# Optimization experiments

Measured on AMD Instinct MI355X. Metric: run time of the kernel, lower is better.

The kernel has to match this reference:

```python
import jax, jax.numpy as jnp
import numpy as np

EPS = 1e-8
TEMPERATURE = 1.0


def setup_inputs() -> dict:
    key = jax.random.key(0)
    basin_seq = jax.random.normal(key, (4, 512, 64), dtype=jnp.float32)
    residual_scale = jnp.ones((), dtype=jnp.float32)  # nn.Parameter(torch.tensor(1.0))
    return {"basin_seq": basin_seq, "residual_scale": residual_scale}


def _project_to_simplex(x):
    sp = jax.nn.softplus(x)
    p = sp / (sp.sum(axis=-1, keepdims=True) + EPS)
    return jnp.maximum(p, EPS)


def _qfi_attention_weights(x, temperature):
    # x: (B, T, D)
    p = _project_to_simplex(x)
    # fisher_rao_distance_simplex re-normalizes both operands
    p = p / (p.sum(axis=-1, keepdims=True) + EPS)
    # Faithful: eps is inside the sqrt, so this is a true (B,T,T,D) reduction,
    # not sqrt(p) @ sqrt(p)^T.
    inner = jnp.sqrt(p[:, :, None, :] * p[:, None, :, :] + EPS).sum(axis=-1)  # (B,T,T)
    inner = jnp.clip(inner, -1.0 + 1e-6, 1.0 - 1e-6)
    dist = 2.0 * jnp.arccos(inner)
    logits = -dist / max(float(temperature), 1e-6)
    return jax.nn.softmax(logits, axis=-1)  # (B,T,T)


def _phi_from_activations(acts):
    # acts: (B, T, D)
    t = acts.shape[1]
    x = acts - acts.mean(axis=1, keepdims=True)
    cov = jnp.einsum('btd,bte->bde', x, x) / (t + EPS)
    var = jnp.maximum(jnp.diagonal(cov, axis1=-2, axis2=-1), EPS)  # (B,D)
    denom = jnp.maximum(jnp.sqrt(var[:, :, None] * var[:, None, :]), EPS)
    corr = jnp.clip(cov / denom, -1.0, 1.0)
    d = corr.shape[-1]
    offdiag = corr * (1.0 - jnp.eye(d, dtype=corr.dtype))
    return jnp.abs(offdiag).mean(axis=(-2, -1))  # (B,)


def _kappa_proxy(x):
    return jnp.linalg.norm(x, axis=-1).mean(axis=-1)  # (B,)


def reference(basin_seq, residual_scale):
    x = basin_seq
    for _ in range(2):
        w = _qfi_attention_weights(x, TEMPERATURE)
        x_attn = jnp.einsum('bij,bjd->bid', w, x)
        x = 0.5 * x + 0.5 * x_attn
        x = x + 0.01 * residual_scale * (x_attn - x)
    phi = _phi_from_activations(x)
    kappa = _kappa_proxy(x)
    return (x, phi, kappa)
```

## Files before the change

kernel.cpp:

```cpp
#include <hip/hip_runtime.h>
#include <math.h>

#define B_ 4
#define T_ 512
#define D_ 64
#define EPS 1e-8f

__device__ __forceinline__ float wave_sum(float v) {
#pragma unroll
  for (int m = 1; m < 64; m <<= 1) v += __shfl_xor(v, m, 64);
  return v;
}
__device__ __forceinline__ float wave_max(float v) {
#pragma unroll
  for (int m = 1; m < 64; m <<= 1) v = fmaxf(v, __shfl_xor(v, m, 64));
  return v;
}
__device__ __forceinline__ float softplus_f(float x) {
  return fmaxf(x, 0.0f) + log1pf(expf(-fabsf(x)));
}

__global__ __launch_bounds__(256) void proj_kernel(const float* __restrict__ x,
                                                   float* __restrict__ s) {
  int wave = threadIdx.x >> 6, lane = threadIdx.x & 63;
  int row = blockIdx.x * 4 + wave;
  float sp = softplus_f(x[row * D_ + lane]);
  float s1 = wave_sum(sp);
  float p = sp / (s1 + EPS);
  p = fmaxf(p, EPS);
  float s2 = wave_sum(p);
  s[row * D_ + lane] = sqrtf(p / (s2 + EPS));
}

__global__ __launch_bounds__(256) void logits_kernel(const float* __restrict__ s,
                                                     float* __restrict__ L) {
  int jt = blockIdx.x, it = blockIdx.y, b = blockIdx.z;
  __shared__ float si[64][68];
  __shared__ float sj[64][68];
  int tid = threadIdx.x;
  const float* sb = s + b * T_ * D_;
#pragma unroll
  for (int k = 0; k < 4; ++k) {
    int idx = tid + k * 256;
    int row = idx >> 4, c4 = idx & 15;
    *(float4*)&si[row][c4 * 4] = *(const float4*)(sb + (it * 64 + row) * D_ + c4 * 4);
    *(float4*)&sj[row][c4 * 4] = *(const float4*)(sb + (jt * 64 + row) * D_ + c4 * 4);
  }
  __syncthreads();

  int i4 = tid >> 4, j4 = tid & 15;
  float acc[4][4];
#pragma unroll
  for (int a = 0; a < 4; ++a)
#pragma unroll
    for (int c = 0; c < 4; ++c) acc[a][c] = 0.f;

#pragma unroll 4
  for (int d4 = 0; d4 < 16; ++d4) {
    float4 A[4], Bv[4];
#pragma unroll
    for (int a = 0; a < 4; ++a) A[a] = *(const float4*)&si[i4 + 16 * a][d4 * 4];
#pragma unroll
    for (int c = 0; c < 4; ++c) Bv[c] = *(const float4*)&sj[j4 + 16 * c][d4 * 4];
#pragma unroll
    for (int a = 0; a < 4; ++a)
#pragma unroll
      for (int c = 0; c < 4; ++c) {
        acc[a][c] = fmaf(A[a].x, Bv[c].x, acc[a][c]);
        acc[a][c] = fmaf(A[a].y, Bv[c].y, acc[a][c]);
        acc[a][c] = fmaf(A[a].z, Bv[c].z, acc[a][c]);
        acc[a][c] = fmaf(A[a].w, Bv[c].w, acc[a][c]);
      }
  }
#pragma unroll
  for (int a = 0; a < 4; ++a) {
    int i = it * 64 + i4 + 16 * a;
    float* Lr = L + ((size_t)(b * T_) + i) * T_ + jt * 64;
#pragma unroll
    for (int c = 0; c < 4; ++c) {
      float inner = fminf(fmaxf(acc[a][c], -1.0f + 1e-6f), 1.0f - 1e-6f);
      Lr[j4 + 16 * c] = -2.0f * acosf(inner);
    }
  }
}

__global__ __launch_bounds__(256) void apply_kernel(const float* __restrict__ L,
                                                    const float* __restrict__ xin,
                                                    const float* __restrict__ rsp,
                                                    float* __restrict__ xout,
                                                    float* __restrict__ sout) {
  int b = blockIdx.y;
  int i0 = blockIdx.x * 8;
  __shared__ float wR[8][512];
  __shared__ float red[4][8][64];
  int tid = threadIdx.x;
  int w = tid >> 6, lane = tid & 63;

#pragma unroll
  for (int r = 0; r < 2; ++r) {
    int i = w * 2 + r;
    const float* Lr = L + ((size_t)(b * T_) + i0 + i) * T_;
    float4 v0 = ((const float4*)Lr)[lane];
    float4 v1 = ((const float4*)Lr)[64 + lane];
    float m = fmaxf(fmaxf(fmaxf(v0.x, v0.y), fmaxf(v0.z, v0.w)),
                    fmaxf(fmaxf(v1.x, v1.y), fmaxf(v1.z, v1.w)));
    m = wave_max(m);
    float4 e0, e1;
    e0.x = __expf(v0.x - m); e0.y = __expf(v0.y - m);
    e0.z = __expf(v0.z - m); e0.w = __expf(v0.w - m);
    e1.x = __expf(v1.x - m); e1.y = __expf(v1.y - m);
    e1.z = __expf(v1.z - m); e1.w = __expf(v1.w - m);
    float ssum = wave_sum(e0.x + e0.y + e0.z + e0.w + e1.x + e1.y + e1.z + e1.w);
    float inv = 1.0f / ssum;
    e0.x *= inv; e0.y *= inv; e0.z *= inv; e0.w *= inv;
    e1.x *= inv; e1.y *= inv; e1.z *= inv; e1.w *= inv;
    *(float4*)&wR[i][lane * 4] = e0;
    *(float4*)&wR[i][256 + lane * 4] = e1;
  }
  __syncthreads();

  int dg = tid & 15, js = tid >> 4;
  float acc[8][4];
#pragma unroll
  for (int i = 0; i < 8; ++i)
#pragma unroll
    for (int k = 0; k < 4; ++k) acc[i][k] = 0.f;

  const float* xb = xin + (size_t)(b * T_) * D_;
#pragma unroll 2
  for (int jj = 0; jj < 8; ++jj) {
    int jbase = jj * 64 + js * 4;
    float xr[4][4];
#pragma unroll
    for (int c = 0; c < 4; ++c) {
      float4 xv = *(const float4*)(xb + (jbase + c) * D_ + dg * 4);
      xr[c][0] = xv.x; xr[c][1] = xv.y; xr[c][2] = xv.z; xr[c][3] = xv.w;
    }
#pragma unroll
    for (int i = 0; i < 8; ++i) {
      float4 wv = *(const float4*)&wR[i][jbase];
      float wc[4] = {wv.x, wv.y, wv.z, wv.w};
#pragma unroll
      for (int c = 0; c < 4; ++c)
#pragma unroll
        for (int k = 0; k < 4; ++k)
          acc[i][k] = fmaf(wc[c], xr[c][k], acc[i][k]);
    }
  }

#pragma unroll
  for (int i = 0; i < 8; ++i)
#pragma unroll
    for (int k = 0; k < 4; ++k) {
      float v = acc[i][k];
      v += __shfl_xor(v, 16, 64);
      v += __shfl_xor(v, 32, 64);
      acc[i][k] = v;
    }
  if (lane < 16) {
#pragma unroll
    for (int i = 0; i < 8; ++i)
      *(float4*)&red[w][i][lane * 4] =
          make_float4(acc[i][0], acc[i][1], acc[i][2], acc[i][3]);
  }
  __syncthreads();

  float c01 = 0.01f * rsp[0];
#pragma unroll
  for (int h = 0; h < 2; ++h) {
    int i = w + 4 * h, d = lane;
    float xa = red[0][i][d] + red[1][i][d] + red[2][i][d] + red[3][i][d];
    size_t idx = ((size_t)(b * T_) + i0 + i) * D_ + d;
    float xn = 0.5f * (1.0f - c01) * xin[idx] + 0.5f * (1.0f + c01) * xa;
    xout[idx] = xn;
    float sp = softplus_f(xn);
    float s1 = wave_sum(sp);
    float p = sp / (s1 + EPS);
    p = fmaxf(p, EPS);
    float s2 = wave_sum(p);
    sout[idx] = sqrtf(p / (s2 + EPS));
  }
}

__global__ __launch_bounds__(256) void p1_kernel(const float* __restrict__ x,
                                                 float* __restrict__ covp,
                                                 float* __restrict__ meanp,
                                                 float* __restrict__ kappap) {
  int blk = blockIdx.x;
  int b = blk >> 3, sl = blk & 7;
  const float* xb = x + ((size_t)(b * T_) + sl * 64) * D_;
  __shared__ float tile[64][68];
  __shared__ float red2[4][64];
  __shared__ float kred[4];
  int tid = threadIdx.x;
#pragma unroll
  for (int k = 0; k < 4; ++k) {
    int idx = tid + k * 256;
    int row = idx >> 4, c4 = idx & 15;
    *(float4*)&tile[row][c4 * 4] = *(const float4*)(xb + row * D_ + c4 * 4);
  }
  __syncthreads();

  {
    int d = tid & 63, q = tid >> 6;
    float ms = 0.f;
#pragma unroll
    for (int tt = 0; tt < 16; ++tt) ms += tile[q * 16 + tt][d];
    red2[q][d] = ms;
  }

  {
    int tr = tid >> 2, qq = tid & 3;
    float ksq = 0.f;
#pragma unroll
    for (int k = 0; k < 16; ++k) {
      float v = tile[tr][qq * 16 + k];
      ksq = fmaf(v, v, ksq);
    }
    ksq += __shfl_xor(ksq, 1, 64);
    ksq += __shfl_xor(ksq, 2, 64);
    float contrib = (qq == 0) ? sqrtf(ksq) : 0.f;
    contrib = wave_sum(contrib);
    if ((tid & 63) == 0) kred[tid >> 6] = contrib;
  }

  int dd = tid >> 2, e16 = tid & 3;
  float acc[16];
#pragma unroll
  for (int k = 0; k < 16; ++k) acc[k] = 0.f;
  for (int tt = 0; tt < 64; ++tt) {
    float xd = tile[tt][dd];
    const float4* te = (const float4*)&tile[tt][e16 * 16];
    float4 v0 = te[0], v1 = te[1], v2 = te[2], v3 = te[3];
    acc[0]  = fmaf(xd, v0.x, acc[0]);  acc[1]  = fmaf(xd, v0.y, acc[1]);
    acc[2]  = fmaf(xd, v0.z, acc[2]);  acc[3]  = fmaf(xd, v0.w, acc[3]);
    acc[4]  = fmaf(xd, v1.x, acc[4]);  acc[5]  = fmaf(xd, v1.y, acc[5]);
    acc[6]  = fmaf(xd, v1.z, acc[6]);  acc[7]  = fmaf(xd, v1.w, acc[7]);
    acc[8]  = fmaf(xd, v2.x, acc[8]);  acc[9]  = fmaf(xd, v2.y, acc[9]);
    acc[10] = fmaf(xd, v2.z, acc[10]); acc[11] = fmaf(xd, v2.w, acc[11]);
    acc[12] = fmaf(xd, v3.x, acc[12]); acc[13] = fmaf(xd, v3.y, acc[13]);
    acc[14] = fmaf(xd, v3.z, acc[14]); acc[15] = fmaf(xd, v3.w, acc[15]);
  }
  float* cp = covp + (size_t)blk * 4096 + dd * 64 + e16 * 16;
#pragma unroll
  for (int kk = 0; kk < 4; ++kk)
    *(float4*)(cp + kk * 4) =
        make_float4(acc[kk * 4], acc[kk * 4 + 1], acc[kk * 4 + 2], acc[kk * 4 + 3]);
  __syncthreads();
  if (tid < 64)
    meanp[blk * 64 + tid] = red2[0][tid] + red2[1][tid] + red2[2][tid] + red2[3][tid];
  if (tid == 0) kappap[blk] = kred[0] + kred[1] + kred[2] + kred[3];
}

__global__ __launch_bounds__(256) void p2_kernel(const float* __restrict__ covp,
                                                 const float* __restrict__ meanp,
                                                 const float* __restrict__ kappap,
                                                 float* __restrict__ out) {
  int b = blockIdx.x;
  __shared__ float mu[64];
  __shared__ float var[64];
  __shared__ float phired[4];
  int tid = threadIdx.x;
  if (tid < 64) {
    float m = 0.f;
#pragma unroll
    for (int s = 0; s < 8; ++s) m += meanp[(b * 8 + s) * 64 + tid];
    mu[tid] = m * (1.0f / 512.0f);
  }
  __syncthreads();

  int dd = tid >> 2, e16 = tid & 3;
  float acc[16];
#pragma unroll
  for (int k = 0; k < 16; ++k) acc[k] = 0.f;
#pragma unroll
  for (int s = 0; s < 8; ++s) {
    const float* cp = covp + (size_t)(b * 8 + s) * 4096 + dd * 64 + e16 * 16;
#pragma unroll
    for (int kk = 0; kk < 4; ++kk) {
      float4 v = *(const float4*)(cp + kk * 4);
      acc[kk * 4] += v.x; acc[kk * 4 + 1] += v.y;
      acc[kk * 4 + 2] += v.z; acc[kk * 4 + 3] += v.w;
    }
  }
  float mud = mu[dd];
#pragma unroll
  for (int k = 0; k < 16; ++k)
    acc[k] = acc[k] * (1.0f / 512.0f) - mud * mu[e16 * 16 + k];
  if ((dd >> 4) == e16) var[dd] = fmaxf(acc[dd & 15], EPS);
  __syncthreads();

  float vd = var[dd];
  float psum = 0.f;
#pragma unroll
  for (int k = 0; k < 16; ++k) {
    int e = e16 * 16 + k;
    if (e == dd) continue;
    float denom = fmaxf(sqrtf(vd * var[e]), EPS);
    float cc = fminf(fmaxf(acc[k] / denom, -1.0f), 1.0f);
    psum += fabsf(cc);
  }
  psum = wave_sum(psum);
  if ((tid & 63) == 0) phired[tid >> 6] = psum;
  __syncthreads();
  if (tid == 0) {
    out[B_ * T_ * D_ + b] = (phired[0] + phired[1] + phired[2] + phired[3]) *
                            (1.0f / 4096.0f);
    float ks = 0.f;
#pragma unroll
    for (int s = 0; s < 8; ++s) ks += kappap[b * 8 + s];
    out[B_ * T_ * D_ + B_ + b] = ks * (1.0f / 512.0f);
  }
}

extern "C" void kernel_launch(void* const* d_in, const int* in_sizes, int n_in,
                              void* d_out, int out_size, void* d_ws, size_t ws_size,
                              hipStream_t stream) {
  const float* x0 = (const float*)d_in[0];
  const float* rs = (const float*)d_in[1];
  float* out = (float*)d_out;
  float* s     = (float*)d_ws;
  float* L     = s + B_ * T_ * D_;
  float* x1    = L + B_ * T_ * T_;
  float* covp  = x1 + B_ * T_ * D_;
  float* meanp = covp + 32 * 4096;
  float* kappap = meanp + 32 * 64;

  dim3 lgrd(8, 8, 4), agrd(64, 4);
  proj_kernel<<<(B_ * T_) / 4, 256, 0, stream>>>(x0, s);
  logits_kernel<<<lgrd, 256, 0, stream>>>(s, L);
  apply_kernel<<<agrd, 256, 0, stream>>>(L, x0, rs, x1, s);
  logits_kernel<<<lgrd, 256, 0, stream>>>(s, L);
  apply_kernel<<<agrd, 256, 0, stream>>>(L, x1, rs, out, s);
  p1_kernel<<<32, 256, 0, stream>>>(out, covp, meanp, kappap);
  p2_kernel<<<4, 256, 0, stream>>>(covp, meanp, kappap, out);
}
```

Baseline: 104.3 us.

## Fuse logits computation into attention apply kernel and fold stats into second pass

Each attention block now computes its own 8x512 logits tile in shared memory and no longer writes or reads the B×T×T logits buffer in global memory. That removes the separate logits launches and their global round-trip. The second attention pass also emits per-block covariance, mean and norm partials, which removes the p1 kernel. In exchange, each block recomputes the s_j loads for the full sequence, only 256 blocks are launched, and p2 must now reduce 64 partials instead of 8. A separate s2 buffer avoids a read/write race on s.

```diff
diff --git a/kernel.cpp b/kernel.cpp
--- a/kernel.cpp
+++ b/kernel.cpp
@@ -32,76 +32,94 @@
   s[row * D_ + lane] = sqrtf(p / (s2 + EPS));
 }
 
-__global__ __launch_bounds__(256) void logits_kernel(const float* __restrict__ s,
-                                                     float* __restrict__ L) {
-  int jt = blockIdx.x, it = blockIdx.y, b = blockIdx.z;
-  __shared__ float si[64][68];
-  __shared__ float sj[64][68];
-  int tid = threadIdx.x;
-  const float* sb = s + b * T_ * D_;
-#pragma unroll
-  for (int k = 0; k < 4; ++k) {
-    int idx = tid + k * 256;
-    int row = idx >> 4, c4 = idx & 15;
-    *(float4*)&si[row][c4 * 4] = *(const float4*)(sb + (it * 64 + row) * D_ + c4 * 4);
-    *(float4*)&sj[row][c4 * 4] = *(const float4*)(sb + (jt * 64 + row) * D_ + c4 * 4);
-  }
-  __syncthreads();
-
-  int i4 = tid >> 4, j4 = tid & 15;
-  float acc[4][4];
-#pragma unroll
-  for (int a = 0; a < 4; ++a)
-#pragma unroll
-    for (int c = 0; c < 4; ++c) acc[a][c] = 0.f;
-
-#pragma unroll 4
-  for (int d4 = 0; d4 < 16; ++d4) {
-    float4 A[4], Bv[4];
-#pragma unroll
-    for (int a = 0; a < 4; ++a) A[a] = *(const float4*)&si[i4 + 16 * a][d4 * 4];
-#pragma unroll
-    for (int c = 0; c < 4; ++c) Bv[c] = *(const float4*)&sj[j4 + 16 * c][d4 * 4];
-#pragma unroll
-    for (int a = 0; a < 4; ++a)
-#pragma unroll
-      for (int c = 0; c < 4; ++c) {
-        acc[a][c] = fmaf(A[a].x, Bv[c].x, acc[a][c]);
-        acc[a][c] = fmaf(A[a].y, Bv[c].y, acc[a][c]);
-        acc[a][c] = fmaf(A[a].z, Bv[c].z, acc[a][c]);
-        acc[a][c] = fmaf(A[a].w, Bv[c].w, acc[a][c]);
-      }
-  }
-#pragma unroll
-  for (int a = 0; a < 4; ++a) {
-    int i = it * 64 + i4 + 16 * a;
-    float* Lr = L + ((size_t)(b * T_) + i) * T_ + jt * 64;
-#pragma unroll
-    for (int c = 0; c < 4; ++c) {
-      float inner = fminf(fmaxf(acc[a][c], -1.0f + 1e-6f), 1.0f - 1e-6f);
-      Lr[j4 + 16 * c] = -2.0f * acosf(inner);
-    }
-  }
-}
-
-__global__ __launch_bounds__(256) void apply_kernel(const float* __restrict__ L,
-                                                    const float* __restrict__ xin,
-                                                    const float* __restrict__ rsp,
-                                                    float* __restrict__ xout,
-                                                    float* __restrict__ sout) {
-  int b = blockIdx.y;
-  int i0 = blockIdx.x * 8;
-  __shared__ float wR[8][512];
-  __shared__ float red[4][8][64];
+template <bool PART>
+__global__ __launch_bounds__(256) void attn_kernel(
+    const float* __restrict__ s_in, const float* __restrict__ x_in,
+    const float* __restrict__ rsp, float* __restrict__ x_out,
+    float* __restrict__ s_out, float* __restrict__ covp,
+    float* __restrict__ meanp, float* __restrict__ kappap) {
+  int b = blockIdx.y, ic = blockIdx.x;
+  int i0 = ic * 8;
+  __shared__ __align__(16) float smem[13352];
+  float* si8 = smem;
+  float* wbuf = smem + 544;
+  float* sj = smem + 4640;
+  float* red = sj;
+  float* xf = sj + 2048;
+  float* kred = sj + 2592;
   int tid = threadIdx.x;
   int w = tid >> 6, lane = tid & 63;
+  const float* sb = s_in + (size_t)b * T_ * D_;
+  const float* xb = x_in + (size_t)b * T_ * D_;
+
+#pragma unroll
+  for (int k = 0; k < 2; ++k) {
+    int idx = tid + k * 256, r = idx >> 6, d = idx & 63;
+    si8[r * 68 + d] = sb[(i0 + r) * D_ + d];
+  }
+  __syncthreads();
+
+  int iq = tid >> 7, jq = (tid >> 2) & 31, ds = tid & 3;
+  float4 Areg[4][4];
+#pragma unroll
+  for (int a = 0; a < 4; ++a)
+#pragma unroll
+    for (int dq = 0; dq < 4; ++dq)
+      Areg[a][dq] = *(const float4*)&si8[(iq * 4 + a) * 68 + ds * 16 + dq * 4];
+
+  for (int c = 0; c < 4; ++c) {
+    __syncthreads();
+#pragma unroll
+    for (int k = 0; k < 8; ++k) {
+      int idx = tid + k * 256, r = idx >> 4, q = idx & 15;
+      *(float4*)&sj[r * 68 + q * 4] =
+          *(const float4*)(sb + (c * 128 + r) * D_ + q * 4);
+    }
+    __syncthreads();
+    float accL[4][4];
+#pragma unroll
+    for (int a = 0; a < 4; ++a)
+#pragma unroll
+      for (int cc = 0; cc < 4; ++cc) accL[a][cc] = 0.f;
+#pragma unroll
+    for (int dq = 0; dq < 4; ++dq) {
+      float4 Bv[4];
+#pragma unroll
+      for (int cc = 0; cc < 4; ++cc)
+        Bv[cc] = *(const float4*)&sj[(jq + 32 * cc) * 68 + ds * 16 + dq * 4];
+#pragma unroll
+      for (int a = 0; a < 4; ++a) {
+        float4 A = Areg[a][dq];
+#pragma unroll
+        for (int cc = 0; cc < 4; ++cc) {
+          accL[a][cc] = fmaf(A.x, Bv[cc].x, accL[a][cc]);
+          accL[a][cc] = fmaf(A.y, Bv[cc].y, accL[a][cc]);
+          accL[a][cc] = fmaf(A.z, Bv[cc].z, accL[a][cc]);
+          accL[a][cc] = fmaf(A.w, Bv[cc].w, accL[a][cc]);
+        }
+      }
+    }
+#pragma unroll
+    for (int a = 0; a < 4; ++a)
+#pragma unroll
+      for (int cc = 0; cc < 4; ++cc) {
+        float v = accL[a][cc];
+        v += __shfl_xor(v, 1, 64);
+        v += __shfl_xor(v, 2, 64);
+        if (ds == 0) {
+          float inner = fminf(fmaxf(v, -1.0f + 1e-6f), 1.0f - 1e-6f);
+          wbuf[(iq * 4 + a) * 512 + c * 128 + jq + 32 * cc] = -2.0f * acosf(inner);
+        }
+      }
+  }
+  __syncthreads();
 
 #pragma unroll
   for (int r = 0; r < 2; ++r) {
     int i = w * 2 + r;
-    const float* Lr = L + ((size_t)(b * T_) + i0 + i) * T_;
-    float4 v0 = ((const float4*)Lr)[lane];
-    float4 v1 = ((const float4*)Lr)[64 + lane];
+    float* Wr = wbuf + i * 512;
+    float4 v0 = ((float4*)Wr)[lane];
+    float4 v1 = ((float4*)Wr)[64 + lane];
     float m = fmaxf(fmaxf(fmaxf(v0.x, v0.y), fmaxf(v0.z, v0.w)),
                     fmaxf(fmaxf(v1.x, v1.y), fmaxf(v1.z, v1.w)));
     m = wave_max(m);
@@ -114,8 +132,8 @@
     float inv = 1.0f / ssum;
     e0.x *= inv; e0.y *= inv; e0.z *= inv; e0.w *= inv;
     e1.x *= inv; e1.y *= inv; e1.z *= inv; e1.w *= inv;
-    *(float4*)&wR[i][lane * 4] = e0;
-    *(float4*)&wR[i][256 + lane * 4] = e1;
+    ((float4*)Wr)[lane] = e0;
+    ((float4*)Wr)[64 + lane] = e1;
   }
   __syncthreads();
 
@@ -125,8 +143,6 @@
   for (int i = 0; i < 8; ++i)
 #pragma unroll
     for (int k = 0; k < 4; ++k) acc[i][k] = 0.f;
-
-  const float* xb = xin + (size_t)(b * T_) * D_;
 #pragma unroll 2
   for (int jj = 0; jj < 8; ++jj) {
     int jbase = jj * 64 + js * 4;
@@ -138,7 +154,7 @@
     }
 #pragma unroll
     for (int i = 0; i < 8; ++i) {
-      float4 wv = *(const float4*)&wR[i][jbase];
+      float4 wv = *(const float4*)&wbuf[i * 512 + jbase];
       float wc[4] = {wv.x, wv.y, wv.z, wv.w};
 #pragma unroll
       for (int c = 0; c < 4; ++c)
@@ -147,7 +163,6 @@
           acc[i][k] = fmaf(wc[c], xr[c][k], acc[i][k]);
     }
   }
-
 #pragma unroll
   for (int i = 0; i < 8; ++i)
 #pragma unroll
@@ -160,96 +175,68 @@
   if (lane < 16) {
 #pragma unroll
     for (int i = 0; i < 8; ++i)
-      *(float4*)&red[w][i][lane * 4] =
+      *(float4*)&red[(w * 8 + i) * 64 + lane * 4] =
           make_float4(acc[i][0], acc[i][1], acc[i][2], acc[i][3]);
   }
   __syncthreads();
 
   float c01 = 0.01f * rsp[0];
+  float kacc = 0.f;
 #pragma unroll
   for (int h = 0; h < 2; ++h) {
     int i = w + 4 * h, d = lane;
-    float xa = red[0][i][d] + red[1][i][d] + red[2][i][d] + red[3][i][d];
+    float xa = red[(0 * 8 + i) * 64 + d] + red[(1 * 8 + i) * 64 + d] +
+               red[(2 * 8 + i) * 64 + d] + red[(3 * 8 + i) * 64 + d];
     size_t idx = ((size_t)(b * T_) + i0 + i) * D_ + d;
-    float xn = 0.5f * (1.0f - c01) * xin[idx] + 0.5f * (1.0f + c01) * xa;
-    xout[idx] = xn;
-    float sp = softplus_f(xn);
-    float s1 = wave_sum(sp);
-    float p = sp / (s1 + EPS);
-    p = fmaxf(p, EPS);
-    float s2 = wave_sum(p);
-    sout[idx] = sqrtf(p / (s2 + EPS));
-  }
-}
-
-__global__ __launch_bounds__(256) void p1_kernel(const float* __restrict__ x,
-                                                 float* __restrict__ covp,
-                                                 float* __restrict__ meanp,
-                                                 float* __restrict__ kappap) {
-  int blk = blockIdx.x;
-  int b = blk >> 3, sl = blk & 7;
-  const float* xb = x + ((size_t)(b * T_) + sl * 64) * D_;
-  __shared__ float tile[64][68];
-  __shared__ float red2[4][64];
-  __shared__ float kred[4];
-  int tid = threadIdx.x;
-#pragma unroll
-  for (int k = 0; k < 4; ++k) {
-    int idx = tid + k * 256;
-    int row = idx >> 4, c4 = idx & 15;
-    *(float4*)&tile[row][c4 * 4] = *(const float4*)(xb + row * D_ + c4 * 4);
-  }
-  __syncthreads();
-
-  {
-    int d = tid & 63, q = tid >> 6;
-    float ms = 0.f;
-#pragma unroll
-    for (int tt = 0; tt < 16; ++tt) ms += tile[q * 16 + tt][d];
-    red2[q][d] = ms;
-  }
-
-  {
-    int tr = tid >> 2, qq = tid & 3;
-    float ksq = 0.f;
-#pragma unroll
-    for (int k = 0; k < 16; ++k) {
-      float v = tile[tr][qq * 16 + k];
-      ksq = fmaf(v, v, ksq);
-    }
-    ksq += __shfl_xor(ksq, 1, 64);
-    ksq += __shfl_xor(ksq, 2, 64);
-    float contrib = (qq == 0) ? sqrtf(ksq) : 0.f;
-    contrib = wave_sum(contrib);
-    if ((tid & 63) == 0) kred[tid >> 6] = contrib;
-  }
-
-  int dd = tid >> 2, e16 = tid & 3;
-  float acc[16];
-#pragma unroll
-  for (int k = 0; k < 16; ++k) acc[k] = 0.f;
-  for (int tt = 0; tt < 64; ++tt) {
-    float xd = tile[tt][dd];
-    const float4* te = (const float4*)&tile[tt][e16 * 16];
-    float4 v0 = te[0], v1 = te[1], v2 = te[2], v3 = te[3];
-    acc[0]  = fmaf(xd, v0.x, acc[0]);  acc[1]  = fmaf(xd, v0.y, acc[1]);
-    acc[2]  = fmaf(xd, v0.z, acc[2]);  acc[3]  = fmaf(xd, v0.w, acc[3]);
-    acc[4]  = fmaf(xd, v1.x, acc[4]);  acc[5]  = fmaf(xd, v1.y, acc[5]);
-    acc[6]  = fmaf(xd, v1.z, acc[6]);  acc[7]  = fmaf(xd, v1.w, acc[7]);
-    acc[8]  = fmaf(xd, v2.x, acc[8]);  acc[9]  = fmaf(xd, v2.y, acc[9]);
-    acc[10] = fmaf(xd, v2.z, acc[10]); acc[11] = fmaf(xd, v2.w, acc[11]);
-    acc[12] = fmaf(xd, v3.x, acc[12]); acc[13] = fmaf(xd, v3.y, acc[13]);
-    acc[14] = fmaf(xd, v3.z, acc[14]); acc[15] = fmaf(xd, v3.w, acc[15]);
-  }
-  float* cp = covp + (size_t)blk * 4096 + dd * 64 + e16 * 16;
-#pragma unroll
-  for (int kk = 0; kk < 4; ++kk)
-    *(float4*)(cp + kk * 4) =
-        make_float4(acc[kk * 4], acc[kk * 4 + 1], acc[kk * 4 + 2], acc[kk * 4 + 3]);
-  __syncthreads();
-  if (tid < 64)
-    meanp[blk * 64 + tid] = red2[0][tid] + red2[1][tid] + red2[2][tid] + red2[3][tid];
-  if (tid == 0) kappap[blk] = kred[0] + kred[1] + kred[2] + kred[3];
+    float xn = 0.5f * (1.0f - c01) * x_in[idx] + 0.5f * (1.0f + c01) * xa;
+    x_out[idx] = xn;
+    if (!PART) {
+      float sp = softplus_f(xn);
+      float s1 = wave_sum(sp);
+      float p = sp / (s1 + EPS);
+      p = fmaxf(p, EPS);
+      float s2 = wave_sum(p);
+      s_out[idx] = sqrtf(p / (s2 + EPS));
+    } else {
+      xf[i * 68 + d] = xn;
+      float ssq = wave_sum(xn * xn);
+      kacc += sqrtf(ssq);
+    }
+  }
+  if (PART) {
+    if (lane == 0) kred[w] = kacc;
+    __syncthreads();
+    int dd = tid >> 2, e16 = tid & 3;
+    float ac[16];
+#pragma unroll
+    for (int k = 0; k < 16; ++k) ac[k] = 0.f;
+#pragma unroll
+    for (int t = 0; t < 8; ++t) {
+      float xd = xf[t * 68 + dd];
+      const float4* te = (const float4*)&xf[t * 68 + e16 * 16];
+      float4 v0 = te[0], v1 = te[1], v2 = te[2], v3 = te[3];
+      ac[0]  = fmaf(xd, v0.x, ac[0]);  ac[1]  = fmaf(xd, v0.y, ac[1]);
+      ac[2]  = fmaf(xd, v0.z, ac[2]);  ac[3]  = fmaf(xd, v0.w, ac[3]);
+      ac[4]  = fmaf(xd, v1.x, ac[4]);  ac[5]  = fmaf(xd, v1.y, ac[5]);
+      ac[6]  = fmaf(xd, v1.z, ac[6]);  ac[7]  = fmaf(xd, v1.w, ac[7]);
+      ac[8]  = fmaf(xd, v2.x, ac[8]);  ac[9]  = fmaf(xd, v2.y, ac[9]);
+      ac[10] = fmaf(xd, v2.z, ac[10]); ac[11] = fmaf(xd, v2.w, ac[11]);
+      ac[12] = fmaf(xd, v3.x, ac[12]); ac[13] = fmaf(xd, v3.y, ac[13]);
+      ac[14] = fmaf(xd, v3.z, ac[14]); ac[15] = fmaf(xd, v3.w, ac[15]);
+    }
+    float* cp = covp + ((size_t)(b * 64 + ic)) * 4096 + dd * 64 + e16 * 16;
+#pragma unroll
+    for (int kk = 0; kk < 4; ++kk)
+      *(float4*)(cp + kk * 4) =
+          make_float4(ac[kk * 4], ac[kk * 4 + 1], ac[kk * 4 + 2], ac[kk * 4 + 3]);
+    if (tid < 64) {
+      float m = 0.f;
+#pragma unroll
+      for (int t = 0; t < 8; ++t) m += xf[t * 68 + tid];
+      meanp[(b * 64 + ic) * 64 + tid] = m;
+    }
+    if (tid == 0) kappap[b * 64 + ic] = kred[0] + kred[1] + kred[2] + kred[3];
+  }
 }
 
 __global__ __launch_bounds__(256) void p2_kernel(const float* __restrict__ covp,
@@ -263,8 +250,7 @@
   int tid = threadIdx.x;
   if (tid < 64) {
     float m = 0.f;
-#pragma unroll
-    for (int s = 0; s < 8; ++s) m += meanp[(b * 8 + s) * 64 + tid];
+    for (int s = 0; s < 64; ++s) m += meanp[(b * 64 + s) * 64 + tid];
     mu[tid] = m * (1.0f / 512.0f);
   }
   __syncthreads();
@@ -273,9 +259,8 @@
   float acc[16];
 #pragma unroll
   for (int k = 0; k < 16; ++k) acc[k] = 0.f;
-#pragma unroll
-  for (int s = 0; s < 8; ++s) {
-    const float* cp = covp + (size_t)(b * 8 + s) * 4096 + dd * 64 + e16 * 16;
+  for (int s = 0; s < 64; ++s) {
+    const float* cp = covp + ((size_t)(b * 64 + s)) * 4096 + dd * 64 + e16 * 16;
 #pragma unroll
     for (int kk = 0; kk < 4; ++kk) {
       float4 v = *(const float4*)(cp + kk * 4);
@@ -307,8 +292,7 @@
     out[B_ * T_ * D_ + b] = (phired[0] + phired[1] + phired[2] + phired[3]) *
                             (1.0f / 4096.0f);
     float ks = 0.f;
-#pragma unroll
-    for (int s = 0; s < 8; ++s) ks += kappap[b * 8 + s];
+    for (int s = 0; s < 64; ++s) ks += kappap[b * 64 + s];
     out[B_ * T_ * D_ + B_ + b] = ks * (1.0f / 512.0f);
   }
 }
@@ -319,19 +303,16 @@
   const float* x0 = (const float*)d_in[0];
   const float* rs = (const float*)d_in[1];
   float* out = (float*)d_out;
-  float* s     = (float*)d_ws;
-  float* L     = s + B_ * T_ * D_;
-  float* x1    = L + B_ * T_ * T_;
-  float* covp  = x1 + B_ * T_ * D_;
-  float* meanp = covp + 32 * 4096;
-  float* kappap = meanp + 32 * 64;
-
-  dim3 lgrd(8, 8, 4), agrd(64, 4);
+  float* s = (float*)d_ws;
+  float* s2 = s + 131072;
+  float* x1 = s2 + 131072;
+  float* covp = x1 + 131072;
+  float* meanp = covp + 256 * 4096;
+  float* kappap = meanp + 256 * 64;
+
+  dim3 agrd(64, B_);
   proj_kernel<<<(B_ * T_) / 4, 256, 0, stream>>>(x0, s);
-  logits_kernel<<<lgrd, 256, 0, stream>>>(s, L);
-  apply_kernel<<<agrd, 256, 0, stream>>>(L, x0, rs, x1, s);
-  logits_kernel<<<lgrd, 256, 0, stream>>>(s, L);
-  apply_kernel<<<agrd, 256, 0, stream>>>(L, x1, rs, out, s);
-  p1_kernel<<<32, 256, 0, stream>>>(out, covp, meanp, kappap);
-  p2_kernel<<<4, 256, 0, stream>>>(covp, meanp, kappap, out);
-}
+  attn_kernel<false><<<agrd, 256, 0, stream>>>(s, x0, rs, x1, s2, covp, meanp, kappap);
+  attn_kernel<true><<<agrd, 256, 0, stream>>>(s2, x1, rs, out, s, covp, meanp, kappap);
+  p2_kernel<<<B_, 256, 0, stream>>>(covp, meanp, kappap, out);
+}
```

Result: slower. 129.4 us (+24.0%).
